# Kernel optimization log

Measured on AMD Instinct MI355X. Metric: run time of the kernel, lower is better.

## Reference

```python
import jax, jax.numpy as jnp
import numpy as np
import math

B, D, S, C, H = 8192, 512, 5, 2048, 4

def setup_inputs() -> dict:
    key = jax.random.key(0)
    ks = jax.random.split(key, 8)
    return {
        "features": jax.random.normal(ks[0], (B, D), dtype=jnp.float32),
        "logits": jax.random.normal(ks[1], (S, B, C), dtype=jnp.float32),
        "scale_feats": jax.random.normal(ks[2], (S, B, D), dtype=jnp.float32),
        "Wq": jax.random.normal(ks[3], (D, D), dtype=jnp.float32) * 0.02,
        "bq": jnp.zeros((D,), jnp.float32),
        "Wk": jax.random.normal(ks[4], (D, D), dtype=jnp.float32) * 0.02,
        "bk": jnp.zeros((D,), jnp.float32),
        "Wv": jax.random.normal(ks[5], (D, D), dtype=jnp.float32) * 0.02,
        "bv": jnp.zeros((D,), jnp.float32),
        "scale_emb": jax.random.normal(ks[6], (S, D), dtype=jnp.float32) * 0.02,
        "temperature": jnp.float32(0.07),
        "attn_w": jnp.ones((3,), jnp.float32) / 3.0,
    }

def reference(features, logits, scale_feats, Wq, bq, Wk, bk, Wv, bv, scale_emb, temperature, attn_w):
    b, d = features.shape
    s = scale_feats.shape[0]
    hd = d // H
    t = jnp.abs(temperature)

    # ---- multihead attention over scales (V is computed in torch but unused) ----
    Q = (features @ Wq + bq).reshape(b, H, hd)                      # [B,H,hd]
    sf_emb = scale_feats + scale_emb[:, None, :]                    # [S,B,D]
    K = (sf_emb @ Wk + bk).reshape(s, b, H, hd)                     # [S,B,H,hd]
    scores = jnp.einsum('bhd,sbhd->bhs', Q, K) / jnp.float32(math.sqrt(hd))
    attn_mha = jax.nn.softmax(scores / t, axis=-1).mean(axis=1)     # [B,S]

    # ---- geometric (angular) attention ----
    fn = features / jnp.linalg.norm(features, axis=-1, keepdims=True).clip(1e-12)
    sfn = scale_feats / jnp.linalg.norm(scale_feats, axis=-1, keepdims=True).clip(1e-12)
    cos_sim = jnp.einsum('bd,sbd->bs', fn, sfn)                     # [B,S]
    angles = jnp.arccos(jnp.clip(cos_sim, -1.0 + 1e-7, 1.0 - 1e-7))
    attn_geo = jax.nn.softmax(jnp.exp(-angles / t), axis=-1)        # [B,S]

    # ---- Cayley-Menger volume-proxy attention ----
    # simplex points: [features, scale_feat, cos(a)*f + sin(a)*s for a in {pi/4, pi/2, 3pi/4}]
    c = jnp.float32(math.sqrt(0.5))
    cf = jnp.array([1.0, 0.0, c, 0.0, -c], jnp.float32)             # coeffs on features
    cs = jnp.array([0.0, 1.0, c, 1.0, c], jnp.float32)              # coeffs on scale_feat
    simplex = (cf[None, :, None, None] * features[None, None] +
               cs[None, :, None, None] * scale_feats[:, None])      # [S,5,B,D]
    norms = jnp.sum(simplex * simplex, axis=-1)                     # [S,5,B]
    gram = jnp.einsum('spbd,sqbd->spqb', simplex, simplex)          # [S,5,5,B]
    distsq = norms[:, :, None] + norms[:, None, :] - 2.0 * gram     # [S,5,5,B]
    volumes = distsq.mean(axis=(1, 2)).T                            # [B,S]
    attn_cay = jax.nn.softmax(volumes / t, axis=-1)

    # ---- fuse attention types ----
    w = jax.nn.softmax(attn_w, axis=0)
    combined = w[0] * attn_mha + w[1] * attn_geo + w[2] * attn_cay  # [B,S]
    combined = combined / combined.sum(axis=-1, keepdims=True)

    combined_logits = jnp.einsum('bs,sbc->bc', combined, logits)    # [B,C]
    return (combined_logits, combined)
```

## Files before the change

### kernel.cpp

```cpp
#include <hip/hip_runtime.h>
#include <math.h>

#define B_N 8192
#define D_N 512
#define S_N 5
#define C_N 2048
#define H_N 4
#define RB 32

typedef __attribute__((ext_vector_type(8))) short bf16x8;
typedef __attribute__((ext_vector_type(4))) float floatx4;

__device__ __forceinline__ float bf2f(short u) {
  union { unsigned int i; float f; } c;
  c.i = ((unsigned int)(unsigned short)u) << 16;
  return c.f;
}
__device__ __forceinline__ short f2bf(float f) {
  union { float f; unsigned int i; } c; c.f = f;
  unsigned int x = c.i;
  x += 0x7fffu + ((x >> 16) & 1u);
  return (short)(x >> 16);
}
__device__ __forceinline__ unsigned long long pack4(float a, float b, float c, float d) {
  return (unsigned long long)(unsigned short)f2bf(a)
       | ((unsigned long long)(unsigned short)f2bf(b) << 16)
       | ((unsigned long long)(unsigned short)f2bf(c) << 32)
       | ((unsigned long long)(unsigned short)f2bf(d) << 48);
}

__global__ __launch_bounds__(256) void k_prep(const float* __restrict__ Wq,
                                              const float* __restrict__ Wk,
                                              short* __restrict__ WqT,
                                              short* __restrict__ Wkb) {
  int o = blockIdx.x * 256 + threadIdx.x;
  if (blockIdx.x < 1024) {
    int n = o >> 9, k = o & 511;
    WqT[(size_t)n * 512 + k] = f2bf(Wq[(size_t)k * 512 + n]);
  } else {
    int o2 = o - 262144;
    Wkb[o2] = f2bf(Wk[o2]);
  }
}

__global__ __launch_bounds__(256, 2) void k_mega(
    const float* __restrict__ f, const float* __restrict__ sf,
    const float* __restrict__ emb, const short* __restrict__ WqT,
    const short* __restrict__ Wkb, const float* __restrict__ bq,
    const float* __restrict__ bk, const float* __restrict__ temp,
    const float* __restrict__ attn_w, float* __restrict__ comb_out) {
  __shared__ __align__(16) short uni[21120];
  __shared__ __align__(16) short Qbf[16384];
  __shared__ float ffLds[RB];
  __shared__ float qtLds[RB][H_N];
  __shared__ float scLds[RB][H_N][S_N];
  __shared__ float fsLds[S_N][RB];
  __shared__ float ssLds[S_N][RB];

  const int tid = threadIdx.x;
  const int lane = tid & 63;
  const int wid = tid >> 6;
  const int b0 = blockIdx.x * RB;

  {
    const int r0 = tid >> 3;
    const int c0 = (tid & 7) * 64;
    const float* fp = f + (size_t)(b0 + r0) * D_N + c0;
    float ffp = 0.0f;
#pragma unroll
    for (int i = 0; i < 8; ++i) {
      floatx4 a = *(const floatx4*)(fp + i * 8);
      floatx4 b = *(const floatx4*)(fp + i * 8 + 4);
      ffp += a[0]*a[0] + a[1]*a[1] + a[2]*a[2] + a[3]*a[3];
      ffp += b[0]*b[0] + b[1]*b[1] + b[2]*b[2] + b[3]*b[3];
      bf16x8 o;
      o[0]=f2bf(a[0]); o[1]=f2bf(a[1]); o[2]=f2bf(a[2]); o[3]=f2bf(a[3]);
      o[4]=f2bf(b[0]); o[5]=f2bf(b[1]); o[6]=f2bf(b[2]); o[7]=f2bf(b[3]);
      int byteoff = (r0 * 1024 + (c0 + i * 8) * 2) ^ ((r0 & 7) << 4);
      *(bf16x8*)((char*)uni + byteoff) = o;
    }
    ffp += __shfl_xor(ffp, 1, 64);
    ffp += __shfl_xor(ffp, 2, 64);
    ffp += __shfl_xor(ffp, 4, 64);
    if ((tid & 7) == 0) ffLds[r0] = ffp;
  }
  __syncthreads();

  {
    const int wcol0 = wid * 128;
    floatx4 acc[2][8];
    const floatx4 zero = {0.f, 0.f, 0.f, 0.f};
#pragma unroll
    for (int m = 0; m < 2; ++m)
#pragma unroll
      for (int n = 0; n < 8; ++n) acc[m][n] = zero;

    for (int ks = 0; ks < 16; ++ks) {
      bf16x8 bfr[8];
#pragma unroll
      for (int n = 0; n < 8; ++n) {
        int col = wcol0 + n * 16 + (lane & 15);
        bfr[n] = *(const bf16x8*)(WqT + (size_t)col * 512 + ks * 32 + (lane >> 4) * 8);
      }
      bf16x8 afr[2];
#pragma unroll
      for (int m = 0; m < 2; ++m) {
        int row = m * 16 + (lane & 15);
        int byteoff = (row * 1024 + (ks * 32 + (lane >> 4) * 8) * 2) ^ ((row & 7) << 4);
        afr[m] = *(const bf16x8*)((const char*)uni + byteoff);
      }
#pragma unroll
      for (int m = 0; m < 2; ++m)
#pragma unroll
        for (int n = 0; n < 8; ++n)
          acc[m][n] = __builtin_amdgcn_mfma_f32_16x16x32_bf16(afr[m], bfr[n], acc[m][n], 0, 0, 0);
    }

    float bqv[8], bkv[8];
#pragma unroll
    for (int n = 0; n < 8; ++n) {
      int col = wcol0 + n * 16 + (lane & 15);
      bqv[n] = bq[col];
      bkv[n] = bk[col];
    }
#pragma unroll
    for (int m = 0; m < 2; ++m) {
#pragma unroll
      for (int j = 0; j < 4; ++j) {
        int row = m * 16 + (lane >> 4) * 4 + j;
        float qp = 0.0f;
#pragma unroll
        for (int n = 0; n < 8; ++n) {
          float qv = acc[m][n][j] + bqv[n];
          int col = wcol0 + n * 16 + (lane & 15);
          int byteoff = (row * 1024 + col * 2) ^ ((row & 7) << 4);
          *(short*)((char*)Qbf + byteoff) = f2bf(qv);
          qp += qv * bkv[n];
        }
        qp += __shfl_xor(qp, 1, 64);
        qp += __shfl_xor(qp, 2, 64);
        qp += __shfl_xor(qp, 4, 64);
        qp += __shfl_xor(qp, 8, 64);
        if ((lane & 15) == 0) qtLds[row][wid] = qp;
      }
    }
  }
  __syncthreads();

  float scp[S_N][2][4];
#pragma unroll
  for (int s = 0; s < S_N; ++s)
#pragma unroll
    for (int m = 0; m < 2; ++m)
#pragma unroll
      for (int j = 0; j < 4; ++j) scp[s][m][j] = 0.0f;
  float ssp[S_N] = {0, 0, 0, 0, 0}, fsp[S_N] = {0, 0, 0, 0, 0};

  const int h = wid;
  for (int cc = 0; cc < 4; ++cc) {
    {
      const int r1 = tid >> 3;
      const int cs0 = (tid & 7) * 16;
      const int ac0 = cc * 128 + cs0;
      const float* fpp = f + (size_t)(b0 + r1) * D_N + ac0;
      float fsl[16];
#pragma unroll
      for (int i = 0; i < 4; ++i) {
        floatx4 v = *(const floatx4*)(fpp + i * 4);
        fsl[i * 4 + 0] = v[0]; fsl[i * 4 + 1] = v[1];
        fsl[i * 4 + 2] = v[2]; fsl[i * 4 + 3] = v[3];
      }
#pragma unroll
      for (int s = 0; s < S_N; ++s) {
        const float* sp = sf + ((size_t)s * B_N + b0 + r1) * D_N + ac0;
        const float* ep = emb + s * D_N + ac0;
        float sv[16], se[16];
#pragma unroll
        for (int i = 0; i < 4; ++i) {
          floatx4 a = *(const floatx4*)(sp + i * 4);
          floatx4 e = *(const floatx4*)(ep + i * 4);
#pragma unroll
          for (int q = 0; q < 4; ++q) {
            sv[i * 4 + q] = a[q];
            se[i * 4 + q] = a[q] + e[q];
          }
        }
        float ssl = 0.0f, fsll = 0.0f;
#pragma unroll
        for (int q = 0; q < 16; ++q) { ssl += sv[q] * sv[q]; fsll += fsl[q] * sv[q]; }
        ssp[s] += ssl; fsp[s] += fsll;
        int rowbase = (s * RB + r1) * 264 + cs0 * 2;
#pragma unroll
        for (int q = 0; q < 4; ++q) {
          unsigned long long pk = pack4(se[q*4], se[q*4+1], se[q*4+2], se[q*4+3]);
          *(unsigned long long*)((char*)uni + rowbase + q * 8) = pk;
        }
      }
    }
    __syncthreads();

    {
      floatx4 acc2[2][8];
      const floatx4 zero = {0.f, 0.f, 0.f, 0.f};
#pragma unroll
      for (int m = 0; m < 2; ++m)
#pragma unroll
        for (int n = 0; n < 8; ++n) acc2[m][n] = zero;

#pragma unroll
      for (int ks = 0; ks < 4; ++ks) {
        bf16x8 bfr[8];
#pragma unroll
        for (int n = 0; n < 8; ++n) {
          int a = cc * 128 + n * 16 + (lane & 15);
          bfr[n] = *(const bf16x8*)(Wkb + (size_t)a * 512 + h * 128 + ks * 32 + (lane >> 4) * 8);
        }
        bf16x8 afr[2];
#pragma unroll
        for (int m = 0; m < 2; ++m) {
          int row = m * 16 + (lane & 15);
          int byteoff = (row * 1024 + (h * 128 + ks * 32 + (lane >> 4) * 8) * 2) ^ ((row & 7) << 4);
          afr[m] = *(const bf16x8*)((const char*)Qbf + byteoff);
        }
#pragma unroll
        for (int m = 0; m < 2; ++m)
#pragma unroll
          for (int n = 0; n < 8; ++n)
            acc2[m][n] = __builtin_amdgcn_mfma_f32_16x16x32_bf16(afr[m], bfr[n], acc2[m][n], 0, 0, 0);
      }
#pragma unroll
      for (int s = 0; s < S_N; ++s) {
#pragma unroll
        for (int m = 0; m < 2; ++m) {
#pragma unroll
          for (int j = 0; j < 4; ++j) {
            int row = m * 16 + (lane >> 4) * 4 + j;
            int base = (s * RB + row) * 264 + (lane & 15) * 2;
            float p = 0.0f;
#pragma unroll
            for (int n = 0; n < 8; ++n) {
              short sv = *(const short*)((const char*)uni + base + n * 32);
              p += acc2[m][n][j] * bf2f(sv);
            }
            scp[s][m][j] += p;
          }
        }
      }
    }
    __syncthreads();
  }

#pragma unroll
  for (int s = 0; s < S_N; ++s)
#pragma unroll
    for (int m = 0; m < 2; ++m)
#pragma unroll
      for (int j = 0; j < 4; ++j) {
        float v = scp[s][m][j];
        v += __shfl_xor(v, 1, 64);
        v += __shfl_xor(v, 2, 64);
        v += __shfl_xor(v, 4, 64);
        v += __shfl_xor(v, 8, 64);
        if ((lane & 15) == 0) scLds[m * 16 + (lane >> 4) * 4 + j][wid][s] = v;
      }
  {
    const int r1 = tid >> 3;
#pragma unroll
    for (int s = 0; s < S_N; ++s) {
      float u = ssp[s], v = fsp[s];
      u += __shfl_xor(u, 1, 64); v += __shfl_xor(v, 1, 64);
      u += __shfl_xor(u, 2, 64); v += __shfl_xor(v, 2, 64);
      u += __shfl_xor(u, 4, 64); v += __shfl_xor(v, 4, 64);
      if ((tid & 7) == 0) { ssLds[s][r1] = u; fsLds[s][r1] = v; }
    }
  }
  __syncthreads();

  if (tid < RB) {
    const int r = tid;
    const float ffv = ffLds[r];
    const float t = fabsf(temp[0]);

    float amha[S_N] = {0, 0, 0, 0, 0};
    const float inv_mha = 1.0f / (sqrtf(128.0f) * t);
#pragma unroll
    for (int hh = 0; hh < H_N; ++hh) {
      float lg[S_N];
#pragma unroll
      for (int s = 0; s < S_N; ++s) lg[s] = (scLds[r][hh][s] + qtLds[r][hh]) * inv_mha;
      float mx = lg[0];
#pragma unroll
      for (int s = 1; s < S_N; ++s) mx = fmaxf(mx, lg[s]);
      float e[S_N], sum = 0;
#pragma unroll
      for (int s = 0; s < S_N; ++s) { e[s] = __expf(lg[s] - mx); sum += e[s]; }
      float isum = 0.25f / sum;
#pragma unroll
      for (int s = 0; s < S_N; ++s) amha[s] += e[s] * isum;
    }

    float ageo[S_N];
    {
      const float nf = fmaxf(sqrtf(ffv), 1e-12f);
      float g[S_N];
#pragma unroll
      for (int s = 0; s < S_N; ++s) {
        float ns = fmaxf(sqrtf(ssLds[s][r]), 1e-12f);
        float cs0 = fsLds[s][r] / (nf * ns);
        cs0 = fminf(fmaxf(cs0, -1.0f + 1e-7f), 1.0f - 1e-7f);
        g[s] = __expf(-acosf(cs0) / t);
      }
      float mx = g[0];
#pragma unroll
      for (int s = 1; s < S_N; ++s) mx = fmaxf(mx, g[s]);
      float sum = 0;
#pragma unroll
      for (int s = 0; s < S_N; ++s) { ageo[s] = __expf(g[s] - mx); sum += ageo[s]; }
#pragma unroll
      for (int s = 0; s < S_N; ++s) ageo[s] /= sum;
    }

    float acay[S_N];
    {
      const float SQ2 = 1.41421356237309515f;
      const float Aff = 0.72f;
      const float Ass = 0.72f - 0.32f * SQ2;
      const float Afs = -(8.0f + 4.0f * SQ2) / 25.0f;
      float lg[S_N];
#pragma unroll
      for (int s = 0; s < S_N; ++s)
        lg[s] = (Aff * ffv + Ass * ssLds[s][r] + Afs * fsLds[s][r]) / t;
      float mx = lg[0];
#pragma unroll
      for (int s = 1; s < S_N; ++s) mx = fmaxf(mx, lg[s]);
      float sum = 0;
#pragma unroll
      for (int s = 0; s < S_N; ++s) { acay[s] = __expf(lg[s] - mx); sum += acay[s]; }
#pragma unroll
      for (int s = 0; s < S_N; ++s) acay[s] /= sum;
    }

    float w0 = attn_w[0], w1 = attn_w[1], w2 = attn_w[2];
    float wm = fmaxf(w0, fmaxf(w1, w2));
    float e0 = __expf(w0 - wm), e1 = __expf(w1 - wm), e2 = __expf(w2 - wm);
    float wsum = e0 + e1 + e2;
    w0 = e0 / wsum; w1 = e1 / wsum; w2 = e2 / wsum;

    float cb[S_N], csum = 0;
#pragma unroll
    for (int s = 0; s < S_N; ++s) {
      cb[s] = w0 * amha[s] + w1 * ageo[s] + w2 * acay[s];
      csum += cb[s];
    }
    float ic = 1.0f / csum;
#pragma unroll
    for (int s = 0; s < S_N; ++s) comb_out[(size_t)(b0 + r) * S_N + s] = cb[s] * ic;
  }
}

__global__ __launch_bounds__(256) void k_mix(const float* __restrict__ logits,
                                             const float* __restrict__ comb,
                                             float* __restrict__ out) {
  const int b = blockIdx.x;
  const int c0 = threadIdx.x * 8;
  float cs[S_N];
#pragma unroll
  for (int s = 0; s < S_N; ++s) cs[s] = comb[(size_t)b * S_N + s];
  floatx4 accA = {0, 0, 0, 0}, accB = {0, 0, 0, 0};
#pragma unroll
  for (int s = 0; s < S_N; ++s) {
    const float* lp = logits + ((size_t)s * B_N + b) * C_N + c0;
    floatx4 lA = *(const floatx4*)lp;
    floatx4 lB = *(const floatx4*)(lp + 4);
    accA += lA * cs[s];
    accB += lB * cs[s];
  }
  float* op = out + (size_t)b * C_N + c0;
  *(floatx4*)op = accA;
  *(floatx4*)(op + 4) = accB;
}

extern "C" void kernel_launch(void* const* d_in, const int* in_sizes, int n_in,
                              void* d_out, int out_size, void* d_ws, size_t ws_size,
                              hipStream_t stream) {
  const float* features = (const float*)d_in[0];
  const float* logits   = (const float*)d_in[1];
  const float* sf       = (const float*)d_in[2];
  const float* Wq       = (const float*)d_in[3];
  const float* bq       = (const float*)d_in[4];
  const float* Wk       = (const float*)d_in[6 - 1];
  const float* bk       = (const float*)d_in[6];
  const float* emb      = (const float*)d_in[9];
  const float* temp     = (const float*)d_in[10];
  const float* attn_w   = (const float*)d_in[11];

  float* out  = (float*)d_out;
  float* comb = out + (size_t)B_N * C_N;

  char* w = (char*)d_ws;
  short* WqT = (short*)(w);
  short* Wkb = (short*)(w + 524288);

  k_prep<<<dim3(2048), dim3(256), 0, stream>>>(Wq, Wk, WqT, Wkb);
  k_mega<<<dim3(256), dim3(256), 0, stream>>>(features, sf, emb, WqT, Wkb, bq, bk,
                                              temp, attn_w, comb);
  k_mix<<<dim3(8192), dim3(256), 0, stream>>>(logits, comb, out);
}
```

Measured before the change: 157.2 us.

## Fuse logit mixing into mega kernel, halve row block, tile weight prep

The separate logits-mixing kernel is folded into the main kernel, so each block mixes the logits for its own rows right after computing the combined weights, and the round trip through global memory plus one launch go away. The row block drops from 32 to 16, doubling the grid to 512 blocks. Features are now kept in LDS as fp32 and reused for the cos-sim pass instead of being reloaded from global. The weight prep kernel now uses an LDS-tiled transpose and vectorized bf16 conversion. The trade-off is that each block does less MFMA work per weight-fragment load, and the heavy streaming of logits now runs inside a kernel limited by LDS occupancy.

```diff
diff --git a/kernel.cpp b/kernel.cpp
--- a/kernel.cpp
+++ b/kernel.cpp
@@ -6,7 +6,7 @@
 #define S_N 5
 #define C_N 2048
 #define H_N 4
-#define RB 32
+#define RB 16
 
 typedef __attribute__((ext_vector_type(8))) short bf16x8;
 typedef __attribute__((ext_vector_type(4))) float floatx4;
@@ -33,13 +33,29 @@
                                               const float* __restrict__ Wk,
                                               short* __restrict__ WqT,
                                               short* __restrict__ Wkb) {
-  int o = blockIdx.x * 256 + threadIdx.x;
-  if (blockIdx.x < 1024) {
-    int n = o >> 9, k = o & 511;
-    WqT[(size_t)n * 512 + k] = f2bf(Wq[(size_t)k * 512 + n]);
+  __shared__ float lds[64][65];
+  const int bx = blockIdx.x, t = threadIdx.x;
+  if (bx < 64) {
+    const int r0 = (bx >> 3) * 64, c0 = (bx & 7) * 64;
+#pragma unroll
+    for (int i = 0; i < 16; ++i) {
+      int r = i * 4 + (t >> 6), c = t & 63;
+      lds[r][c] = Wq[(size_t)(r0 + r) * 512 + c0 + c];
+    }
+    __syncthreads();
+#pragma unroll
+    for (int i = 0; i < 16; ++i) {
+      int cL = i * 4 + (t >> 6), rL = t & 63;
+      WqT[(size_t)(c0 + cL) * 512 + r0 + rL] = f2bf(lds[rL][cL]);
+    }
   } else {
-    int o2 = o - 262144;
-    Wkb[o2] = f2bf(Wk[o2]);
+    const int base = (bx - 64) * 8192 + t * 4;
+#pragma unroll
+    for (int i = 0; i < 8; ++i) {
+      int idx = base + i * 1024;
+      floatx4 v = *(const floatx4*)(Wk + idx);
+      *(unsigned long long*)(Wkb + idx) = pack4(v[0], v[1], v[2], v[3]);
+    }
   }
 }
 
@@ -47,53 +63,53 @@
     const float* __restrict__ f, const float* __restrict__ sf,
     const float* __restrict__ emb, const short* __restrict__ WqT,
     const short* __restrict__ Wkb, const float* __restrict__ bq,
-    const float* __restrict__ bk, const float* __restrict__ temp,
-    const float* __restrict__ attn_w, float* __restrict__ comb_out) {
-  __shared__ __align__(16) short uni[21120];
-  __shared__ __align__(16) short Qbf[16384];
+    const float* __restrict__ bk, const float* __restrict__ logits,
+    const float* __restrict__ temp, const float* __restrict__ attn_w,
+    float* __restrict__ out, float* __restrict__ comb_out) {
+  __shared__ __align__(16) float fLds[RB * 512];
+  __shared__ __align__(16) short Qbf[RB * 512];
+  __shared__ __align__(16) short sfe[S_N * RB * 132];
   __shared__ float ffLds[RB];
   __shared__ float qtLds[RB][H_N];
   __shared__ float scLds[RB][H_N][S_N];
   __shared__ float fsLds[S_N][RB];
   __shared__ float ssLds[S_N][RB];
+  __shared__ float combLds[RB][S_N];
 
   const int tid = threadIdx.x;
   const int lane = tid & 63;
   const int wid = tid >> 6;
   const int b0 = blockIdx.x * RB;
+  const floatx4 fz = {0.f, 0.f, 0.f, 0.f};
 
   {
-    const int r0 = tid >> 3;
-    const int c0 = (tid & 7) * 64;
+    const int r0 = tid >> 4;
+    const int c0 = (tid & 15) * 32;
     const float* fp = f + (size_t)(b0 + r0) * D_N + c0;
+    char* fb = (char*)fLds;
     float ffp = 0.0f;
 #pragma unroll
     for (int i = 0; i < 8; ++i) {
-      floatx4 a = *(const floatx4*)(fp + i * 8);
-      floatx4 b = *(const floatx4*)(fp + i * 8 + 4);
-      ffp += a[0]*a[0] + a[1]*a[1] + a[2]*a[2] + a[3]*a[3];
-      ffp += b[0]*b[0] + b[1]*b[1] + b[2]*b[2] + b[3]*b[3];
-      bf16x8 o;
-      o[0]=f2bf(a[0]); o[1]=f2bf(a[1]); o[2]=f2bf(a[2]); o[3]=f2bf(a[3]);
-      o[4]=f2bf(b[0]); o[5]=f2bf(b[1]); o[6]=f2bf(b[2]); o[7]=f2bf(b[3]);
-      int byteoff = (r0 * 1024 + (c0 + i * 8) * 2) ^ ((r0 & 7) << 4);
-      *(bf16x8*)((char*)uni + byteoff) = o;
+      floatx4 v = *(const floatx4*)(fp + i * 4);
+      ffp += v[0]*v[0] + v[1]*v[1] + v[2]*v[2] + v[3]*v[3];
+      int bo = (r0 * 2048 + (c0 + i * 4) * 4) ^ ((r0 & 7) << 4);
+      *(floatx4*)(fb + bo) = v;
     }
     ffp += __shfl_xor(ffp, 1, 64);
     ffp += __shfl_xor(ffp, 2, 64);
     ffp += __shfl_xor(ffp, 4, 64);
-    if ((tid & 7) == 0) ffLds[r0] = ffp;
+    ffp += __shfl_xor(ffp, 8, 64);
+    if ((tid & 15) == 0) ffLds[r0] = ffp;
   }
   __syncthreads();
 
   {
     const int wcol0 = wid * 128;
-    floatx4 acc[2][8];
-    const floatx4 zero = {0.f, 0.f, 0.f, 0.f};
-#pragma unroll
-    for (int m = 0; m < 2; ++m)
-#pragma unroll
-      for (int n = 0; n < 8; ++n) acc[m][n] = zero;
+    floatx4 acc[8];
+#pragma unroll
+    for (int n = 0; n < 8; ++n) acc[n] = fz;
+    const char* fb = (const char*)fLds;
+    const int row = lane & 15;
 
     for (int ks = 0; ks < 16; ++ks) {
       bf16x8 bfr[8];
@@ -102,18 +118,17 @@
         int col = wcol0 + n * 16 + (lane & 15);
         bfr[n] = *(const bf16x8*)(WqT + (size_t)col * 512 + ks * 32 + (lane >> 4) * 8);
       }
-      bf16x8 afr[2];
-#pragma unroll
-      for (int m = 0; m < 2; ++m) {
-        int row = m * 16 + (lane & 15);
-        int byteoff = (row * 1024 + (ks * 32 + (lane >> 4) * 8) * 2) ^ ((row & 7) << 4);
-        afr[m] = *(const bf16x8*)((const char*)uni + byteoff);
-      }
-#pragma unroll
-      for (int m = 0; m < 2; ++m)
-#pragma unroll
-        for (int n = 0; n < 8; ++n)
-          acc[m][n] = __builtin_amdgcn_mfma_f32_16x16x32_bf16(afr[m], bfr[n], acc[m][n], 0, 0, 0);
+      int kbase = ks * 32 + (lane >> 4) * 8;
+      int bo0 = (row * 2048 + kbase * 4) ^ ((row & 7) << 4);
+      int bo1 = (row * 2048 + kbase * 4 + 16) ^ ((row & 7) << 4);
+      floatx4 a0 = *(const floatx4*)(fb + bo0);
+      floatx4 a1 = *(const floatx4*)(fb + bo1);
+      bf16x8 afr;
+      afr[0] = f2bf(a0[0]); afr[1] = f2bf(a0[1]); afr[2] = f2bf(a0[2]); afr[3] = f2bf(a0[3]);
+      afr[4] = f2bf(a1[0]); afr[5] = f2bf(a1[1]); afr[6] = f2bf(a1[2]); afr[7] = f2bf(a1[3]);
+#pragma unroll
+      for (int n = 0; n < 8; ++n)
+        acc[n] = __builtin_amdgcn_mfma_f32_16x16x32_bf16(afr, bfr[n], acc[n], 0, 0, 0);
     }
 
     float bqv[8], bkv[8];
@@ -124,89 +139,72 @@
       bkv[n] = bk[col];
     }
 #pragma unroll
-    for (int m = 0; m < 2; ++m) {
-#pragma unroll
-      for (int j = 0; j < 4; ++j) {
-        int row = m * 16 + (lane >> 4) * 4 + j;
-        float qp = 0.0f;
-#pragma unroll
-        for (int n = 0; n < 8; ++n) {
-          float qv = acc[m][n][j] + bqv[n];
-          int col = wcol0 + n * 16 + (lane & 15);
-          int byteoff = (row * 1024 + col * 2) ^ ((row & 7) << 4);
-          *(short*)((char*)Qbf + byteoff) = f2bf(qv);
-          qp += qv * bkv[n];
-        }
-        qp += __shfl_xor(qp, 1, 64);
-        qp += __shfl_xor(qp, 2, 64);
-        qp += __shfl_xor(qp, 4, 64);
-        qp += __shfl_xor(qp, 8, 64);
-        if ((lane & 15) == 0) qtLds[row][wid] = qp;
-      }
+    for (int j = 0; j < 4; ++j) {
+      int orow = (lane >> 4) * 4 + j;
+      float qp = 0.0f;
+#pragma unroll
+      for (int n = 0; n < 8; ++n) {
+        float qv = acc[n][j] + bqv[n];
+        int col = wcol0 + n * 16 + (lane & 15);
+        int bo = (orow * 1024 + col * 2) ^ ((orow & 7) << 4);
+        *(short*)((char*)Qbf + bo) = f2bf(qv);
+        qp += qv * bkv[n];
+      }
+      qp += __shfl_xor(qp, 1, 64);
+      qp += __shfl_xor(qp, 2, 64);
+      qp += __shfl_xor(qp, 4, 64);
+      qp += __shfl_xor(qp, 8, 64);
+      if ((lane & 15) == 0) qtLds[orow][wid] = qp;
     }
   }
   __syncthreads();
 
-  float scp[S_N][2][4];
+  float scp[S_N][4];
 #pragma unroll
   for (int s = 0; s < S_N; ++s)
 #pragma unroll
-    for (int m = 0; m < 2; ++m)
-#pragma unroll
-      for (int j = 0; j < 4; ++j) scp[s][m][j] = 0.0f;
+    for (int j = 0; j < 4; ++j) scp[s][j] = 0.0f;
   float ssp[S_N] = {0, 0, 0, 0, 0}, fsp[S_N] = {0, 0, 0, 0, 0};
 
   const int h = wid;
   for (int cc = 0; cc < 4; ++cc) {
     {
-      const int r1 = tid >> 3;
-      const int cs0 = (tid & 7) * 16;
+      const int r1 = tid >> 4;
+      const int cs0 = (tid & 15) * 8;
       const int ac0 = cc * 128 + cs0;
-      const float* fpp = f + (size_t)(b0 + r1) * D_N + ac0;
-      float fsl[16];
-#pragma unroll
-      for (int i = 0; i < 4; ++i) {
-        floatx4 v = *(const floatx4*)(fpp + i * 4);
-        fsl[i * 4 + 0] = v[0]; fsl[i * 4 + 1] = v[1];
-        fsl[i * 4 + 2] = v[2]; fsl[i * 4 + 3] = v[3];
-      }
+      const char* fb = (const char*)fLds;
+      int bo0 = (r1 * 2048 + ac0 * 4) ^ ((r1 & 7) << 4);
+      int bo1 = (r1 * 2048 + ac0 * 4 + 16) ^ ((r1 & 7) << 4);
+      floatx4 f0 = *(const floatx4*)(fb + bo0);
+      floatx4 f1 = *(const floatx4*)(fb + bo1);
+      float fv[8] = {f0[0], f0[1], f0[2], f0[3], f1[0], f1[1], f1[2], f1[3]};
 #pragma unroll
       for (int s = 0; s < S_N; ++s) {
         const float* sp = sf + ((size_t)s * B_N + b0 + r1) * D_N + ac0;
+        floatx4 s0 = *(const floatx4*)(sp);
+        floatx4 s1 = *(const floatx4*)(sp + 4);
         const float* ep = emb + s * D_N + ac0;
-        float sv[16], se[16];
-#pragma unroll
-        for (int i = 0; i < 4; ++i) {
-          floatx4 a = *(const floatx4*)(sp + i * 4);
-          floatx4 e = *(const floatx4*)(ep + i * 4);
-#pragma unroll
-          for (int q = 0; q < 4; ++q) {
-            sv[i * 4 + q] = a[q];
-            se[i * 4 + q] = a[q] + e[q];
-          }
-        }
-        float ssl = 0.0f, fsll = 0.0f;
-#pragma unroll
-        for (int q = 0; q < 16; ++q) { ssl += sv[q] * sv[q]; fsll += fsl[q] * sv[q]; }
-        ssp[s] += ssl; fsp[s] += fsll;
+        floatx4 e0 = *(const floatx4*)(ep);
+        floatx4 e1 = *(const floatx4*)(ep + 4);
+        float sv[8] = {s0[0], s0[1], s0[2], s0[3], s1[0], s1[1], s1[2], s1[3]};
+        float se[8] = {s0[0]+e0[0], s0[1]+e0[1], s0[2]+e0[2], s0[3]+e0[3],
+                       s1[0]+e1[0], s1[1]+e1[1], s1[2]+e1[2], s1[3]+e1[3]};
+        float ssl = 0.0f, fsl = 0.0f;
+#pragma unroll
+        for (int q = 0; q < 8; ++q) { ssl += sv[q] * sv[q]; fsl += fv[q] * sv[q]; }
+        ssp[s] += ssl; fsp[s] += fsl;
         int rowbase = (s * RB + r1) * 264 + cs0 * 2;
-#pragma unroll
-        for (int q = 0; q < 4; ++q) {
-          unsigned long long pk = pack4(se[q*4], se[q*4+1], se[q*4+2], se[q*4+3]);
-          *(unsigned long long*)((char*)uni + rowbase + q * 8) = pk;
-        }
+        *(unsigned long long*)((char*)sfe + rowbase)     = pack4(se[0], se[1], se[2], se[3]);
+        *(unsigned long long*)((char*)sfe + rowbase + 8) = pack4(se[4], se[5], se[6], se[7]);
       }
     }
     __syncthreads();
 
     {
-      floatx4 acc2[2][8];
-      const floatx4 zero = {0.f, 0.f, 0.f, 0.f};
-#pragma unroll
-      for (int m = 0; m < 2; ++m)
-#pragma unroll
-        for (int n = 0; n < 8; ++n) acc2[m][n] = zero;
-
+      floatx4 acc2[8];
+#pragma unroll
+      for (int n = 0; n < 8; ++n) acc2[n] = fz;
+      const int row = lane & 15;
 #pragma unroll
       for (int ks = 0; ks < 4; ++ks) {
         bf16x8 bfr[8];
@@ -215,36 +213,26 @@
           int a = cc * 128 + n * 16 + (lane & 15);
           bfr[n] = *(const bf16x8*)(Wkb + (size_t)a * 512 + h * 128 + ks * 32 + (lane >> 4) * 8);
         }
-        bf16x8 afr[2];
-#pragma unroll
-        for (int m = 0; m < 2; ++m) {
-          int row = m * 16 + (lane & 15);
-          int byteoff = (row * 1024 + (h * 128 + ks * 32 + (lane >> 4) * 8) * 2) ^ ((row & 7) << 4);
-          afr[m] = *(const bf16x8*)((const char*)Qbf + byteoff);
+        int bo = (row * 1024 + (h * 128 + ks * 32 + (lane >> 4) * 8) * 2) ^ ((row & 7) << 4);
+        bf16x8 afr = *(const bf16x8*)((const char*)Qbf + bo);
+#pragma unroll
+        for (int n = 0; n < 8; ++n)
+          acc2[n] = __builtin_amdgcn_mfma_f32_16x16x32_bf16(afr, bfr[n], acc2[n], 0, 0, 0);
+      }
+#pragma unroll
+      for (int s = 0; s < S_N; ++s) {
+#pragma unroll
+        for (int j = 0; j < 4; ++j) {
+          int orow = (lane >> 4) * 4 + j;
+          int base = (s * RB + orow) * 264 + (lane & 15) * 2;
+          float p = 0.0f;
+#pragma unroll
+          for (int n = 0; n < 8; ++n) {
+            short svv = *(const short*)((const char*)sfe + base + n * 32);
+            p += acc2[n][j] * bf2f(svv);
+          }
+          scp[s][j] += p;
         }
-#pragma unroll
-        for (int m = 0; m < 2; ++m)
-#pragma unroll
-          for (int n = 0; n < 8; ++n)
-            acc2[m][n] = __builtin_amdgcn_mfma_f32_16x16x32_bf16(afr[m], bfr[n], acc2[m][n], 0, 0, 0);
-      }
-#pragma unroll
-      for (int s = 0; s < S_N; ++s) {
-#pragma unroll
-        for (int m = 0; m < 2; ++m) {
-#pragma unroll
-          for (int j = 0; j < 4; ++j) {
-            int row = m * 16 + (lane >> 4) * 4 + j;
-            int base = (s * RB + row) * 264 + (lane & 15) * 2;
-            float p = 0.0f;
-#pragma unroll
-            for (int n = 0; n < 8; ++n) {
-              short sv = *(const short*)((const char*)uni + base + n * 32);
-              p += acc2[m][n][j] * bf2f(sv);
-            }
-            scp[s][m][j] += p;
-          }
-        }
       }
     }
     __syncthreads();
@@ -253,25 +241,24 @@
 #pragma unroll
   for (int s = 0; s < S_N; ++s)
 #pragma unroll
-    for (int m = 0; m < 2; ++m)
-#pragma unroll
-      for (int j = 0; j < 4; ++j) {
-        float v = scp[s][m][j];
-        v += __shfl_xor(v, 1, 64);
-        v += __shfl_xor(v, 2, 64);
-        v += __shfl_xor(v, 4, 64);
-        v += __shfl_xor(v, 8, 64);
-        if ((lane & 15) == 0) scLds[m * 16 + (lane >> 4) * 4 + j][wid][s] = v;
-      }
+    for (int j = 0; j < 4; ++j) {
+      float v = scp[s][j];
+      v += __shfl_xor(v, 1, 64);
+      v += __shfl_xor(v, 2, 64);
+      v += __shfl_xor(v, 4, 64);
+      v += __shfl_xor(v, 8, 64);
+      if ((lane & 15) == 0) scLds[(lane >> 4) * 4 + j][wid][s] = v;
+    }
   {
-    const int r1 = tid >> 3;
+    const int r1 = tid >> 4;
 #pragma unroll
     for (int s = 0; s < S_N; ++s) {
       float u = ssp[s], v = fsp[s];
       u += __shfl_xor(u, 1, 64); v += __shfl_xor(v, 1, 64);
       u += __shfl_xor(u, 2, 64); v += __shfl_xor(v, 2, 64);
       u += __shfl_xor(u, 4, 64); v += __shfl_xor(v, 4, 64);
-      if ((tid & 7) == 0) { ssLds[s][r1] = u; fsLds[s][r1] = v; }
+      u += __shfl_xor(u, 8, 64); v += __shfl_xor(v, 8, 64);
+      if ((tid & 15) == 0) { ssLds[s][r1] = u; fsLds[s][r1] = v; }
     }
   }
   __syncthreads();
@@ -354,30 +341,39 @@
     }
     float ic = 1.0f / csum;
 #pragma unroll
-    for (int s = 0; s < S_N; ++s) comb_out[(size_t)(b0 + r) * S_N + s] = cb[s] * ic;
-  }
-}
-
-__global__ __launch_bounds__(256) void k_mix(const float* __restrict__ logits,
-                                             const float* __restrict__ comb,
-                                             float* __restrict__ out) {
-  const int b = blockIdx.x;
-  const int c0 = threadIdx.x * 8;
-  float cs[S_N];
-#pragma unroll
-  for (int s = 0; s < S_N; ++s) cs[s] = comb[(size_t)b * S_N + s];
-  floatx4 accA = {0, 0, 0, 0}, accB = {0, 0, 0, 0};
-#pragma unroll
-  for (int s = 0; s < S_N; ++s) {
-    const float* lp = logits + ((size_t)s * B_N + b) * C_N + c0;
-    floatx4 lA = *(const floatx4*)lp;
-    floatx4 lB = *(const floatx4*)(lp + 4);
-    accA += lA * cs[s];
-    accB += lB * cs[s];
-  }
-  float* op = out + (size_t)b * C_N + c0;
-  *(floatx4*)op = accA;
-  *(floatx4*)(op + 4) = accB;
+    for (int s = 0; s < S_N; ++s) {
+      float cv = cb[s] * ic;
+      combLds[r][s] = cv;
+      comb_out[(size_t)(b0 + r) * S_N + s] = cv;
+    }
+  }
+  __syncthreads();
+
+  {
+    const int c0 = tid * 8;
+#pragma unroll 2
+    for (int r = 0; r < RB; r += 2) {
+      float cA[S_N], cB[S_N];
+#pragma unroll
+      for (int s = 0; s < S_N; ++s) { cA[s] = combLds[r][s]; cB[s] = combLds[r + 1][s]; }
+      floatx4 aA = fz, aB = fz, bA = fz, bB = fz;
+#pragma unroll
+      for (int s = 0; s < S_N; ++s) {
+        const float* lpA = logits + ((size_t)s * B_N + b0 + r) * C_N + c0;
+        floatx4 xA0 = *(const floatx4*)(lpA);
+        floatx4 xA1 = *(const floatx4*)(lpA + 4);
+        floatx4 xB0 = *(const floatx4*)(lpA + C_N);
+        floatx4 xB1 = *(const floatx4*)(lpA + C_N + 4);
+        aA += xA0 * cA[s]; aB += xA1 * cA[s];
+        bA += xB0 * cB[s]; bB += xB1 * cB[s];
+      }
+      float* opA = out + (size_t)(b0 + r) * C_N + c0;
+      *(floatx4*)(opA) = aA;
+      *(floatx4*)(opA + 4) = aB;
+      *(floatx4*)(opA + C_N) = bA;
+      *(floatx4*)(opA + C_N + 4) = bB;
+    }
+  }
 }
 
 extern "C" void kernel_launch(void* const* d_in, const int* in_sizes, int n_in,
@@ -388,7 +384,7 @@
   const float* sf       = (const float*)d_in[2];
   const float* Wq       = (const float*)d_in[3];
   const float* bq       = (const float*)d_in[4];
-  const float* Wk       = (const float*)d_in[6 - 1];
+  const float* Wk       = (const float*)d_in[5];
   const float* bk       = (const float*)d_in[6];
   const float* emb      = (const float*)d_in[9];
   const float* temp     = (const float*)d_in[10];
@@ -401,8 +397,7 @@
   short* WqT = (short*)(w);
   short* Wkb = (short*)(w + 524288);
 
-  k_prep<<<dim3(2048), dim3(256), 0, stream>>>(Wq, Wk, WqT, Wkb);
-  k_mega<<<dim3(256), dim3(256), 0, stream>>>(features, sf, emb, WqT, Wkb, bq, bk,
-                                              temp, attn_w, comb);
-  k_mix<<<dim3(8192), dim3(256), 0, stream>>>(logits, comb, out);
-}
+  k_prep<<<dim3(96), dim3(256), 0, stream>>>(Wq, Wk, WqT, Wkb);
+  k_mega<<<dim3(512), dim3(256), 0, stream>>>(features, sf, emb, WqT, Wkb, bq, bk,
+                                              logits, temp, attn_w, out, comb);
+}
```

Measured after the change: 169.7 us. +8.0%, slower.
